# Kernel optimization log

Hardware: AMD Instinct MI355X
Metric: run time of the kernel (lower is better)

Reference implementation:

```python
import jax, jax.numpy as jnp
import numpy as np

HID = 1024
NH = 16
HD = HID // NH  # 64


def _lin_params(key, fan_in, fan_out):
    k1, k2 = jax.random.split(key)
    lim = 1.0 / np.sqrt(fan_in)
    W = jax.random.uniform(k1, (fan_in, fan_out), jnp.float32, -lim, lim)
    b = jax.random.uniform(k2, (fan_out,), jnp.float32, -lim, lim)
    return W, b


def setup_inputs() -> dict:
    key = jax.random.key(0)
    ks = jax.random.split(key, 12)
    B, S = 4, 1024
    inp = {
        'query': jax.random.normal(ks[0], (B, S, HID), jnp.float32),
        'key': jax.random.normal(ks[1], (B, S, HID), jnp.float32),
        'value': jax.random.normal(ks[2], (B, S, HID), jnp.float32),
    }
    inp['Wq'], inp['bq'] = _lin_params(ks[3], HID, HID)
    inp['Wk'], inp['bk'] = _lin_params(ks[4], HID, HID)
    inp['Wv'], inp['bv'] = _lin_params(ks[5], HID, HID)
    inp['Wp'], inp['bp'] = _lin_params(ks[6], HID, HID)
    inp['Wup'], inp['bup'] = _lin_params(ks[7], HD, 1)
    inp['Wud'], inp['bud'] = _lin_params(ks[8], HD, 1)
    inp['Wus'], inp['bus'] = _lin_params(ks[9], HID, NH)
    inp['Wo'], inp['bo'] = _lin_params(ks[10], HID, HID)
    return inp


def _split_heads(x, B, S):
    # [B,S,HID] -> [B,NH,S,HD]
    return x.reshape(B, S, NH, HD).transpose(0, 2, 1, 3)


def reference(query, key, value, Wq, bq, Wk, bk, Wv, bv, Wp, bp,
              Wup, bup, Wud, bud, Wus, bus, Wo, bo):
    B, S, _ = query.shape
    len_q = S

    q = query @ Wq + bq   # [B,S,HID]
    k = key @ Wk + bk
    v = value @ Wv + bv

    # Gaussian-window positional bias (per head, per query position)
    p = _split_heads(q @ Wp + bp, B, S)              # [B,NH,S,HD]
    tp = jnp.tanh(p)
    p_i = tp @ Wup + bup                             # [B,NH,S,1]
    z_i = tp @ Wud + bud                             # [B,NH,S,1]
    cen_pos = len_q * jax.nn.sigmoid(p_i)            # [B,NH,S,1]
    win_size = len_q * jax.nn.sigmoid(z_i)           # [B,NH,S,1]
    pos = jnp.arange(len_q, dtype=q.dtype)[None, None, None, :]  # [1,1,1,S]
    bias = (pos - cen_pos) ** 2 / (0.5 * win_size ** 2)          # [B,NH,S,S]

    # per-head alpha gate from raw query
    alpha = jax.nn.sigmoid(query @ Wus + bus)        # [B,S,NH]
    alpha = alpha.reshape(B, S, NH, 1).transpose(0, 2, 1, 3)  # [B,NH,S,1]

    qh = _split_heads(q, B, S)
    kh = _split_heads(k, B, S)
    vh = _split_heads(v, B, S)

    scale = 1.0 / jnp.sqrt(jnp.asarray(HD, q.dtype))
    scores = jnp.einsum('bhqd,bhkd->bhqk', qh, kh) * scale
    scores = scores - alpha * bias                   # inject gated Gaussian bias
    attn = jax.nn.softmax(scores, axis=-1)           # [B,NH,S,S]

    out = jnp.einsum('bhqk,bhkd->bhqd', attn, vh)    # [B,NH,S,HD]
    x = out.transpose(0, 2, 1, 3).reshape(B, S, HID)
    x = x @ Wo + bo
    return x, attn
```

## Files before the change

### kernel.cpp

```cpp
#include <hip/hip_runtime.h>
#include <hip/hip_bf16.h>
#include <math.h>

#define S_LEN 1024
#define HIDN  1024
#define NHEAD 16
#define HDIM  64
#define BATCH 4
#define MTOT  (BATCH * S_LEN)

typedef __attribute__((ext_vector_type(8))) short          bf16v8;
typedef __attribute__((ext_vector_type(8))) unsigned short u16v8;
typedef __attribute__((ext_vector_type(4))) unsigned short u16v4;
typedef __attribute__((ext_vector_type(4))) float          f32v4;

__device__ __forceinline__ unsigned short f2bf_rne(float x) {
    unsigned int u = __float_as_uint(x);
    unsigned int r = (u + 0x7fffu + ((u >> 16) & 1u)) >> 16;
    return (unsigned short)r;
}
__device__ __forceinline__ float bf2f(unsigned short h) {
    return __uint_as_float(((unsigned int)h) << 16);
}
__device__ __forceinline__ void split2(float x, unsigned short& h, unsigned short& l) {
    h = f2bf_rne(x);
    l = f2bf_rne(x - bf2f(h));
}

__global__ __launch_bounds__(256) void split_a(
    const float* __restrict__ X, unsigned short* __restrict__ H,
    unsigned short* __restrict__ L)
{
    const int i = blockIdx.x * 256 + threadIdx.x;
    const float4 x0 = ((const float4*)X)[2 * i];
    const float4 x1 = ((const float4*)X)[2 * i + 1];
    float xs[8] = {x0.x, x0.y, x0.z, x0.w, x1.x, x1.y, x1.z, x1.w};
    u16v8 h, l;
#pragma unroll
    for (int j = 0; j < 8; ++j) {
        unsigned short hh, ll;
        split2(xs[j], hh, ll);
        h[j] = hh; l[j] = ll;
    }
    ((u16v8*)H)[i] = h;
    ((u16v8*)L)[i] = l;
}

__global__ __launch_bounds__(256) void split_w(
    const float* __restrict__ W, unsigned short* __restrict__ H,
    unsigned short* __restrict__ L)
{
    __shared__ float T[64][65];
    const int t  = threadIdx.x;
    const int k0 = blockIdx.y * 64;
    const int n0 = blockIdx.x * 64;

    const int r = t >> 4;
    const int c = (t & 15) * 4;
#pragma unroll
    for (int i = 0; i < 4; ++i) {
        const int rr = r + i * 16;
        const float4 v = *(const float4*)&W[(size_t)(k0 + rr) * 1024 + n0 + c];
        T[rr][c + 0] = v.x; T[rr][c + 1] = v.y;
        T[rr][c + 2] = v.z; T[rr][c + 3] = v.w;
    }
    __syncthreads();

    const int n  = t >> 2;
    const int ko = (t & 3) * 16;
    u16v8 h0, h1, l0, l1;
#pragma unroll
    for (int kk = 0; kk < 8; ++kk) {
        unsigned short hh, ll;
        split2(T[ko + kk][n], hh, ll);
        h0[kk] = hh; l0[kk] = ll;
    }
#pragma unroll
    for (int kk = 0; kk < 8; ++kk) {
        unsigned short hh, ll;
        split2(T[ko + 8 + kk][n], hh, ll);
        h1[kk] = hh; l1[kk] = ll;
    }
    unsigned short* Hp = &H[(size_t)(n0 + n) * 1024 + k0 + ko];
    unsigned short* Lp = &L[(size_t)(n0 + n) * 1024 + k0 + ko];
    *(u16v8*)(Hp)     = h0;
    *(u16v8*)(Hp + 8) = h1;
    *(u16v8*)(Lp)     = l0;
    *(u16v8*)(Lp + 8) = l1;
}

__global__ __launch_bounds__(256) void gemm_bf16x3(
    const unsigned short* __restrict__ Ah, const unsigned short* __restrict__ Al,
    const unsigned short* __restrict__ Bh, const unsigned short* __restrict__ Bl,
    const float* __restrict__ bias, float* __restrict__ Cf,
    unsigned short* __restrict__ Ch, unsigned short* __restrict__ Cl, int vt)
{
    __shared__ short Ash[128][40];
    __shared__ short Asl[128][40];
    __shared__ short Bsh[128][40];
    __shared__ short Bsl[128][40];

    const int t    = threadIdx.x;
    const int bm   = blockIdx.y * 128;
    const int bn   = blockIdx.x * 128;
    const int lane = t & 63;
    const int w    = t >> 6;
    const int wr   = w >> 1;
    const int wc   = w & 1;
    const int fr   = lane & 15;
    const int fq   = lane >> 4;
    const int ks   = fq * 8;

    f32v4 zero = {0.f, 0.f, 0.f, 0.f};
    f32v4 acc[4][4];
#pragma unroll
    for (int i = 0; i < 4; ++i)
#pragma unroll
        for (int j = 0; j < 4; ++j) acc[i][j] = zero;

    const int sr = t >> 1;
    const int sc = (t & 1) * 16;
    const unsigned short* pAh = &Ah[(size_t)(bm + sr) * 1024 + sc];
    const unsigned short* pAl = &Al[(size_t)(bm + sr) * 1024 + sc];
    const unsigned short* pBh = &Bh[(size_t)(bn + sr) * 1024 + sc];
    const unsigned short* pBl = &Bl[(size_t)(bn + sr) * 1024 + sc];

    u16v8 rah0, rah1, ral0, ral1, rbh0, rbh1, rbl0, rbl1;
    auto LOAD = [&](int k0) {
        rah0 = *(const u16v8*)(pAh + k0);
        rah1 = *(const u16v8*)(pAh + k0 + 8);
        ral0 = *(const u16v8*)(pAl + k0);
        ral1 = *(const u16v8*)(pAl + k0 + 8);
        rbh0 = *(const u16v8*)(pBh + k0);
        rbh1 = *(const u16v8*)(pBh + k0 + 8);
        rbl0 = *(const u16v8*)(pBl + k0);
        rbl1 = *(const u16v8*)(pBl + k0 + 8);
    };

    LOAD(0);
    for (int k0 = 0; k0 < 1024; k0 += 32) {
        __syncthreads();
        *(u16v8*)&Ash[sr][sc]     = rah0;
        *(u16v8*)&Ash[sr][sc + 8] = rah1;
        *(u16v8*)&Asl[sr][sc]     = ral0;
        *(u16v8*)&Asl[sr][sc + 8] = ral1;
        *(u16v8*)&Bsh[sr][sc]     = rbh0;
        *(u16v8*)&Bsh[sr][sc + 8] = rbh1;
        *(u16v8*)&Bsl[sr][sc]     = rbl0;
        *(u16v8*)&Bsl[sr][sc + 8] = rbl1;
        __syncthreads();

        if (k0 + 32 < 1024) LOAD(k0 + 32);

        bf16v8 fah[4], fal[4], fbh[4], fbl[4];
#pragma unroll
        for (int i = 0; i < 4; ++i) {
            fah[i] = *(const bf16v8*)&Ash[wr * 64 + i * 16 + fr][ks];
            fal[i] = *(const bf16v8*)&Asl[wr * 64 + i * 16 + fr][ks];
            fbh[i] = *(const bf16v8*)&Bsh[wc * 64 + i * 16 + fr][ks];
            fbl[i] = *(const bf16v8*)&Bsl[wc * 64 + i * 16 + fr][ks];
        }
#pragma unroll
        for (int i = 0; i < 4; ++i)
#pragma unroll
            for (int j = 0; j < 4; ++j) {
                acc[i][j] = __builtin_amdgcn_mfma_f32_16x16x32_bf16(
                    fah[i], fbh[j], acc[i][j], 0, 0, 0);
                acc[i][j] = __builtin_amdgcn_mfma_f32_16x16x32_bf16(
                    fah[i], fbl[j], acc[i][j], 0, 0, 0);
                acc[i][j] = __builtin_amdgcn_mfma_f32_16x16x32_bf16(
                    fal[i], fbh[j], acc[i][j], 0, 0, 0);
            }
    }

#pragma unroll
    for (int j = 0; j < 4; ++j) {
        const int col = bn + wc * 64 + j * 16 + fr;
        const float bb = bias[col];
#pragma unroll
        for (int i = 0; i < 4; ++i) {
            const int row0 = bm + wr * 64 + i * 16 + fq * 4;
            const f32v4 cv = acc[i][j];
            if (vt) {
                u16v4 h4, l4;
#pragma unroll
                for (int r = 0; r < 4; ++r) {
                    unsigned short hh, ll;
                    split2(cv[r] + bb, hh, ll);
                    h4[r] = hh; l4[r] = ll;
                }
                const size_t base =
                    ((size_t)((row0 >> 10) * 16 + (col >> 6)) * 64 + (col & 63)) * 1024
                    + (row0 & 1023);
                *(u16v4*)&Ch[base] = h4;
                *(u16v4*)&Cl[base] = l4;
            } else {
#pragma unroll
                for (int r = 0; r < 4; ++r) {
                    const float v = cv[r] + bb;
                    const size_t idx = (size_t)(row0 + r) * 1024 + col;
                    if (Cf) Cf[idx] = v;
                    if (Ch) {
                        unsigned short hh, ll;
                        split2(v, hh, ll);
                        Ch[idx] = hh; Cl[idx] = ll;
                    }
                }
            }
        }
    }
}

__global__ __launch_bounds__(256) void alpha_kernel(
    const float* __restrict__ X, const float* __restrict__ Wus,
    const float* __restrict__ bus, float* __restrict__ alpha)
{
    __shared__ float Ws[1024 * 16];
    const int t = threadIdx.x;
#pragma unroll
    for (int i = 0; i < 16; ++i) {
        const int idx = t + i * 256;
        *reinterpret_cast<float4*>(&Ws[idx * 4]) =
            *reinterpret_cast<const float4*>(&Wus[idx * 4]);
    }
    __syncthreads();

    const int r = t >> 4, c = t & 15;
    const size_t row = (size_t)blockIdx.x * 16 + r;
    const float* x = &X[row * 1024];
    float acc = 0.f;
    for (int kk = 0; kk < 1024; kk += 4) {
        const float4 xv = *reinterpret_cast<const float4*>(&x[kk]);
        acc = fmaf(xv.x, Ws[(kk + 0) * 16 + c], acc);
        acc = fmaf(xv.y, Ws[(kk + 1) * 16 + c], acc);
        acc = fmaf(xv.z, Ws[(kk + 2) * 16 + c], acc);
        acc = fmaf(xv.w, Ws[(kk + 3) * 16 + c], acc);
    }
    acc += bus[c];
    alpha[row * 16 + c] = 1.f / (1.f + expf(-acc));
}

__global__ __launch_bounds__(256) void posparam_kernel(
    const float* __restrict__ p, const float* __restrict__ alpha,
    const float* __restrict__ Wup, const float* __restrict__ bup,
    const float* __restrict__ Wud, const float* __restrict__ bud,
    float* __restrict__ cen, float* __restrict__ c0)
{
    __shared__ float wu[64], wd[64];
    const int t = threadIdx.x;
    if (t < 64) { wu[t] = Wup[t]; wd[t] = Wud[t]; }
    __syncthreads();

    const int tid = blockIdx.x * 256 + t;
    const int b = tid >> 14;
    const int h = (tid >> 10) & 15;
    const int s = tid & 1023;

    const float* pr = &p[((size_t)(b * 1024 + s)) * 1024 + h * 64];
    float ap = 0.f, az = 0.f;
#pragma unroll
    for (int d = 0; d < 64; d += 4) {
        const float4 pv = *reinterpret_cast<const float4*>(&pr[d]);
        const float t0 = tanhf(pv.x), t1 = tanhf(pv.y);
        const float t2 = tanhf(pv.z), t3 = tanhf(pv.w);
        ap += t0 * wu[d] + t1 * wu[d + 1] + t2 * wu[d + 2] + t3 * wu[d + 3];
        az += t0 * wd[d] + t1 * wd[d + 1] + t2 * wd[d + 2] + t3 * wd[d + 3];
    }
    ap += bup[0];
    az += bud[0];
    const float cenv = 1024.f / (1.f + expf(-ap));
    const float win  = 1024.f / (1.f + expf(-az));
    const float al   = alpha[(size_t)(b * 1024 + s) * 16 + h];
    const int oi = (b * 16 + h) * 1024 + s;
    cen[oi] = cenv;
    c0[oi]  = al * 2.f / (win * win);
}

#define M0_SHIFT 8.0f
__global__ __launch_bounds__(256, 2) void attn_fused(
    const unsigned short* __restrict__ qh, const unsigned short* __restrict__ ql,
    const unsigned short* __restrict__ kh, const unsigned short* __restrict__ kl,
    const unsigned short* __restrict__ vTh, const unsigned short* __restrict__ vTl,
    const float* __restrict__ cen, const float* __restrict__ c0,
    float* __restrict__ attn,
    unsigned short* __restrict__ oh, unsigned short* __restrict__ ol)
{
    __shared__ unsigned short KH[64][64], KL[64][64];
    __shared__ unsigned short VH[64][64], VL[64][64];
    __shared__ unsigned short PH[128][64], PL[128][64];
    __shared__ float CEN[128], C0S[128];
    __shared__ float LSUM[2][128];
    __shared__ float RINV[128];

    const int bid   = blockIdx.x;
    const int z     = ((bid >> 6) << 3) | (bid & 7);
    const int itile = (bid >> 3) & 7;
    const int i0    = itile * 128;
    const int bq    = z >> 4;
    const int hd    = z & 15;

    const int t    = threadIdx.x;
    const int lane = t & 63;
    const int w    = t >> 6;
    const int wr   = w >> 1, wc = w & 1;
    const int fr   = lane & 15, fq = lane >> 4;

    if (t < 128) {
        CEN[t] = cen[(size_t)z * 1024 + i0 + t];
        C0S[t] = c0[(size_t)z * 1024 + i0 + t];
    }

    bf16v8 qfh_[4][2], qfl_[4][2];
#pragma unroll
    for (int i = 0; i < 4; ++i)
#pragma unroll
        for (int kk = 0; kk < 2; ++kk) {
            const size_t qa = (size_t)(bq * 1024 + i0 + wr * 64 + i * 16 + fr) * 1024
                              + hd * 64 + kk * 32 + fq * 8;
            qfh_[i][kk] = *(const bf16v8*)&qh[qa];
            qfl_[i][kk] = *(const bf16v8*)&ql[qa];
        }

    float lsum[4][4];
#pragma unroll
    for (int i = 0; i < 4; ++i)
#pragma unroll
        for (int r = 0; r < 4; ++r) lsum[i][r] = 0.f;

    const f32v4 zero = {0.f, 0.f, 0.f, 0.f};

    for (int jt = 0; jt < 16; ++jt) {
        const int j0 = jt * 64;
        __syncthreads();
#pragma unroll
        for (int pp = 0; pp < 2; ++pp) {
            const int c   = t + pp * 256;
            const int row = c >> 3;
            const int seg = c & 7;
            const size_t ga = (size_t)(bq * 1024 + j0 + row) * 1024 + hd * 64 + seg * 8;
            const int sl = (seg ^ (row & 7)) * 8;
            *(u16v8*)&KH[row][sl] = *(const u16v8*)&kh[ga];
            *(u16v8*)&KL[row][sl] = *(const u16v8*)&kl[ga];
        }
        __syncthreads();

        f32v4 acc[4][2];
#pragma unroll
        for (int i = 0; i < 4; ++i)
#pragma unroll
            for (int j2 = 0; j2 < 2; ++j2) acc[i][j2] = zero;

#pragma unroll
        for (int kk = 0; kk < 2; ++kk) {
            bf16v8 fbh[2], fbl[2];
#pragma unroll
            for (int j2 = 0; j2 < 2; ++j2) {
                const int rb = wc * 32 + j2 * 16 + fr;
                const int sb = ((kk * 4 + fq) ^ (rb & 7)) * 8;
                fbh[j2] = *(const bf16v8*)&KH[rb][sb];
                fbl[j2] = *(const bf16v8*)&KL[rb][sb];
            }
#pragma unroll
            for (int i = 0; i < 4; ++i)
#pragma unroll
                for (int j2 = 0; j2 < 2; ++j2) {
                    acc[i][j2] = __builtin_amdgcn_mfma_f32_16x16x32_bf16(
                        qfh_[i][kk], fbh[j2], acc[i][j2], 0, 0, 0);
                    acc[i][j2] = __builtin_amdgcn_mfma_f32_16x16x32_bf16(
                        qfh_[i][kk], fbl[j2], acc[i][j2], 0, 0, 0);
                    acc[i][j2] = __builtin_amdgcn_mfma_f32_16x16x32_bf16(
                        qfl_[i][kk], fbh[j2], acc[i][j2], 0, 0, 0);
                }
        }

#pragma unroll
        for (int i = 0; i < 4; ++i)
#pragma unroll
            for (int r = 0; r < 4; ++r) {
                const int row = wr * 64 + i * 16 + fq * 4 + r;
                const float cv = CEN[row], cc = C0S[row];
                float al = 0.f;
#pragma unroll
                for (int j2 = 0; j2 < 2; ++j2) {
                    const int col = wc * 32 + j2 * 16 + fr;
                    const float dd = (float)(j0 + col) - cv;
                    const float s  = acc[i][j2][r] * 0.125f - cc * dd * dd;
                    al += __expf(s - M0_SHIFT);
                }
                lsum[i][r] += al;
            }
    }

#pragma unroll
    for (int i = 0; i < 4; ++i)
#pragma unroll
        for (int r = 0; r < 4; ++r) {
            float v = lsum[i][r];
            v += __shfl_xor(v, 1);
            v += __shfl_xor(v, 2);
            v += __shfl_xor(v, 4);
            v += __shfl_xor(v, 8);
            if (fr == 0) LSUM[wc][wr * 64 + i * 16 + fq * 4 + r] = v;
        }
    __syncthreads();
    if (t < 128) RINV[t] = 1.f / (LSUM[0][t] + LSUM[1][t]);

    f32v4 acco[4][2];
#pragma unroll
    for (int i = 0; i < 4; ++i)
#pragma unroll
        for (int j = 0; j < 2; ++j) acco[i][j] = zero;

    float* attnZ = attn + (size_t)z * 1024 * 1024;
    const unsigned short* vhb = vTh + (size_t)z * 64 * 1024;
    const unsigned short* vlb = vTl + (size_t)z * 64 * 1024;

    for (int jt = 0; jt < 16; ++jt) {
        const int j0 = jt * 64;
        __syncthreads();
#pragma unroll
        for (int pp = 0; pp < 2; ++pp) {
            const int c   = t + pp * 256;
            const int row = c >> 3;
            const int seg = c & 7;
            const size_t ga = (size_t)(bq * 1024 + j0 + row) * 1024 + hd * 64 + seg * 8;
            const int sl = (seg ^ (row & 7)) * 8;
            *(u16v8*)&KH[row][sl] = *(const u16v8*)&kh[ga];
            *(u16v8*)&KL[row][sl] = *(const u16v8*)&kl[ga];
            const size_t va = (size_t)row * 1024 + j0 + seg * 8;
            *(u16v8*)&VH[row][sl] = *(const u16v8*)&vhb[va];
            *(u16v8*)&VL[row][sl] = *(const u16v8*)&vlb[va];
        }
        __syncthreads();

        f32v4 acc[4][2];
#pragma unroll
        for (int i = 0; i < 4; ++i)
#pragma unroll
            for (int j2 = 0; j2 < 2; ++j2) acc[i][j2] = zero;

#pragma unroll
        for (int kk = 0; kk < 2; ++kk) {
            bf16v8 fbh[2], fbl[2];
#pragma unroll
            for (int j2 = 0; j2 < 2; ++j2) {
                const int rb = wc * 32 + j2 * 16 + fr;
                const int sb = ((kk * 4 + fq) ^ (rb & 7)) * 8;
                fbh[j2] = *(const bf16v8*)&KH[rb][sb];
                fbl[j2] = *(const bf16v8*)&KL[rb][sb];
            }
#pragma unroll
            for (int i = 0; i < 4; ++i)
#pragma unroll
                for (int j2 = 0; j2 < 2; ++j2) {
                    acc[i][j2] = __builtin_amdgcn_mfma_f32_16x16x32_bf16(
                        qfh_[i][kk], fbh[j2], acc[i][j2], 0, 0, 0);
                    acc[i][j2] = __builtin_amdgcn_mfma_f32_16x16x32_bf16(
                        qfh_[i][kk], fbl[j2], acc[i][j2], 0, 0, 0);
                    acc[i][j2] = __builtin_amdgcn_mfma_f32_16x16x32_bf16(
                        qfl_[i][kk], fbh[j2], acc[i][j2], 0, 0, 0);
                }
        }

#pragma unroll
        for (int i = 0; i < 4; ++i)
#pragma unroll
            for (int r = 0; r < 4; ++r) {
                const int row = wr * 64 + i * 16 + fq * 4 + r;
                const float cv = CEN[row], cc = C0S[row], ri = RINV[row];
#pragma unroll
                for (int j2 = 0; j2 < 2; ++j2) {
                    const int col = wc * 32 + j2 * 16 + fr;
                    const float dd = (float)(j0 + col) - cv;
                    const float s  = acc[i][j2][r] * 0.125f - cc * dd * dd;
                    const float p  = __expf(s - M0_SHIFT) * ri;
                    attnZ[(size_t)(i0 + row) * 1024 + j0 + col] = p;
                    unsigned short hv, lv;
                    split2(p, hv, lv);
                    const int slot = ((col >> 3) ^ (row & 7)) * 8 + (col & 7);
                    PH[row][slot] = hv;
                    PL[row][slot] = lv;
                }
            }
        __syncthreads();

#pragma unroll
        for (int kk = 0; kk < 2; ++kk) {
            bf16v8 pah[4], pal[4], fbh[2], fbl[2];
#pragma unroll
            for (int iq = 0; iq < 4; ++iq) {
                const int rp = wr * 64 + iq * 16 + fr;
                const int sp = ((kk * 4 + fq) ^ (rp & 7)) * 8;
                pah[iq] = *(const bf16v8*)&PH[rp][sp];
                pal[iq] = *(const bf16v8*)&PL[rp][sp];
            }
#pragma unroll
            for (int jd = 0; jd < 2; ++jd) {
                const int rb = wc * 32 + jd * 16 + fr;
                const int sb = ((kk * 4 + fq) ^ (rb & 7)) * 8;
                fbh[jd] = *(const bf16v8*)&VH[rb][sb];
                fbl[jd] = *(const bf16v8*)&VL[rb][sb];
            }
#pragma unroll
            for (int iq = 0; iq < 4; ++iq)
#pragma unroll
                for (int jd = 0; jd < 2; ++jd) {
                    acco[iq][jd] = __builtin_amdgcn_mfma_f32_16x16x32_bf16(
                        pah[iq], fbh[jd], acco[iq][jd], 0, 0, 0);
                    acco[iq][jd] = __builtin_amdgcn_mfma_f32_16x16x32_bf16(
                        pah[iq], fbl[jd], acco[iq][jd], 0, 0, 0);
                    acco[iq][jd] = __builtin_amdgcn_mfma_f32_16x16x32_bf16(
                        pal[iq], fbh[jd], acco[iq][jd], 0, 0, 0);
                }
        }
    }

#pragma unroll
    for (int jd = 0; jd < 2; ++jd) {
        const int dcol = wc * 32 + jd * 16 + fr;
#pragma unroll
        for (int iq = 0; iq < 4; ++iq) {
            const int row0 = i0 + wr * 64 + iq * 16 + fq * 4;
            const f32v4 cv = acco[iq][jd];
#pragma unroll
            for (int r = 0; r < 4; ++r) {
                unsigned short hv, lv;
                split2(cv[r], hv, lv);
                const size_t idx = (size_t)(bq * 1024 + row0 + r) * 1024 + hd * 64 + dcol;
                oh[idx] = hv;
                ol[idx] = lv;
            }
        }
    }
}

extern "C" void kernel_launch(void* const* d_in, const int* in_sizes, int n_in,
                              void* d_out, int out_size, void* d_ws, size_t ws_size,
                              hipStream_t stream)
{
    const float* query = (const float*)d_in[0];
    const float* key_  = (const float*)d_in[1];
    const float* value = (const float*)d_in[2];
    const float* Wq  = (const float*)d_in[3];
    const float* bq  = (const float*)d_in[4];
    const float* Wk  = (const float*)d_in[5];
    const float* bk  = (const float*)d_in[6];
    const float* Wv  = (const float*)d_in[7];
    const float* bv  = (const float*)d_in[8];
    const float* Wp  = (const float*)d_in[9];
    const float* bp  = (const float*)d_in[10];
    const float* Wup = (const float*)d_in[11];
    const float* bup = (const float*)d_in[12];
    const float* Wud = (const float*)d_in[13];
    const float* bud = (const float*)d_in[14];
    const float* Wus = (const float*)d_in[15];
    const float* bus = (const float*)d_in[16];
    const float* Wo  = (const float*)d_in[17];
    const float* bo  = (const float*)d_in[18];

    float* x_out = (float*)d_out;
    float* attn  = x_out + (size_t)MTOT * HIDN;

    char* wsb = (char*)d_ws;
    unsigned short* qh  = (unsigned short*)(wsb);
    unsigned short* ql  = (unsigned short*)(wsb + (8u  << 20));
    unsigned short* kh  = (unsigned short*)(wsb + (16u << 20));
    unsigned short* kl  = (unsigned short*)(wsb + (24u << 20));
    unsigned short* vTh = (unsigned short*)(wsb + (32u << 20));
    unsigned short* vTl = (unsigned short*)(wsb + (40u << 20));
    float* p_ws  = (float*)(wsb + (48u << 20));
    unsigned short* oh = (unsigned short*)(wsb + (48u << 20));
    unsigned short* ol = (unsigned short*)(wsb + (56u << 20));
    float* alpha_ws = (float*)(wsb + (64u << 20));
    float* cen_ws   = (float*)(wsb + (64u << 20) + (256u << 10));
    float* c0_ws    = (float*)(wsb + (64u << 20) + (512u << 10));
    unsigned short* ah = (unsigned short*)attn;
    unsigned short* al = ah + (size_t)MTOT * HIDN;
    unsigned short* wh = al + (size_t)MTOT * HIDN;
    unsigned short* wl = wh + (size_t)HIDN * HIDN;
    unsigned short* w2h = qh;
    unsigned short* w2l = ql;

    const dim3 blk(256);
    const dim3 gsplit_a(MTOT * HIDN / 8 / 256);
    const dim3 gsplit_w(16, 16);
    const dim3 ggemm(HIDN / 128, MTOT / 128);

    split_w<<<gsplit_w, blk, 0, stream>>>(Wq, wh, wl);
    split_a<<<gsplit_a, blk, 0, stream>>>(query, ah, al);
    gemm_bf16x3<<<ggemm, blk, 0, stream>>>(ah, al, wh, wl, bq, nullptr, qh, ql, 0);
    split_w<<<gsplit_w, blk, 0, stream>>>(Wk, wh, wl);
    split_a<<<gsplit_a, blk, 0, stream>>>(key_, ah, al);
    gemm_bf16x3<<<ggemm, blk, 0, stream>>>(ah, al, wh, wl, bk, nullptr, kh, kl, 0);
    split_w<<<gsplit_w, blk, 0, stream>>>(Wv, wh, wl);
    split_a<<<gsplit_a, blk, 0, stream>>>(value, ah, al);
    gemm_bf16x3<<<ggemm, blk, 0, stream>>>(ah, al, wh, wl, bv, nullptr, vTh, vTl, 1);
    split_w<<<gsplit_w, blk, 0, stream>>>(Wp, wh, wl);
    gemm_bf16x3<<<ggemm, blk, 0, stream>>>(qh, ql, wh, wl, bp, p_ws, nullptr, nullptr, 0);
    alpha_kernel<<<dim3(MTOT / 16), blk, 0, stream>>>(query, Wus, bus, alpha_ws);
    posparam_kernel<<<dim3((BATCH * NHEAD * S_LEN) / 256), blk, 0, stream>>>(
        p_ws, alpha_ws, Wup, bup, Wud, bud, cen_ws, c0_ws);
    attn_fused<<<dim3(512), blk, 0, stream>>>(
        qh, ql, kh, kl, vTh, vTl, cen_ws, c0_ws, attn, oh, ol);
    split_w<<<gsplit_w, blk, 0, stream>>>(Wo, w2h, w2l);
    gemm_bf16x3<<<ggemm, blk, 0, stream>>>(oh, ol, w2h, w2l, bo, x_out,
                                           nullptr, nullptr, 0);
}
```

Measured before the change: 440.6 us.

## Compute transposed score tiles per wave to keep softmax rows in registers

Reorganizes the attention kernel so each wave owns 32 query rows and computes S^T = K·Q^T, putting each query row in a lane. Row sums then need only two cross-lane shuffles, with no shared-memory LSUM/RINV/CEN staging or block syncs for the softmax. The P tile stays in a per-wave LDS slice, which removes a block-wide barrier before P·V, and attention probabilities and outputs are written as float4/u16v4 vectors. The shared-memory cut permits raising launch bounds to 3 blocks per SM, at the cost of more register pressure and different store coalescing patterns.

New measurement: 456.2 us. 1.04x slower.

```diff
diff --git a/kernel.cpp b/kernel.cpp
--- a/kernel.cpp
+++ b/kernel.cpp
@@ -277,7 +277,7 @@
 }
 
 #define M0_SHIFT 8.0f
-__global__ __launch_bounds__(256, 2) void attn_fused(
+__global__ __launch_bounds__(256, 3) void attn_fused(
     const unsigned short* __restrict__ qh, const unsigned short* __restrict__ ql,
     const unsigned short* __restrict__ kh, const unsigned short* __restrict__ kl,
     const unsigned short* __restrict__ vTh, const unsigned short* __restrict__ vTl,
@@ -287,10 +287,7 @@
 {
     __shared__ unsigned short KH[64][64], KL[64][64];
     __shared__ unsigned short VH[64][64], VL[64][64];
-    __shared__ unsigned short PH[128][64], PL[128][64];
-    __shared__ float CEN[128], C0S[128];
-    __shared__ float LSUM[2][128];
-    __shared__ float RINV[128];
+    __shared__ unsigned short PTH[4][16][64], PTL[4][16][64];
 
     const int bid   = blockIdx.x;
     const int z     = ((bid >> 6) << 3) | (bid & 7);
@@ -302,32 +299,30 @@
     const int t    = threadIdx.x;
     const int lane = t & 63;
     const int w    = t >> 6;
-    const int wr   = w >> 1, wc = w & 1;
     const int fr   = lane & 15, fq = lane >> 4;
-
-    if (t < 128) {
-        CEN[t] = cen[(size_t)z * 1024 + i0 + t];
-        C0S[t] = c0[(size_t)z * 1024 + i0 + t];
-    }
-
-    bf16v8 qfh_[4][2], qfl_[4][2];
-#pragma unroll
-    for (int i = 0; i < 4; ++i)
+    const int q0w  = w * 32;
+
+    float cenq[2], c0q[2];
+#pragma unroll
+    for (int n2 = 0; n2 < 2; ++n2) {
+        const size_t ix = (size_t)z * 1024 + i0 + q0w + n2 * 16 + fr;
+        cenq[n2] = cen[ix];
+        c0q[n2]  = c0[ix];
+    }
+
+    bf16v8 qfh_[2][2], qfl_[2][2];
+#pragma unroll
+    for (int n2 = 0; n2 < 2; ++n2)
 #pragma unroll
         for (int kk = 0; kk < 2; ++kk) {
-            const size_t qa = (size_t)(bq * 1024 + i0 + wr * 64 + i * 16 + fr) * 1024
+            const size_t qa = (size_t)(bq * 1024 + i0 + q0w + n2 * 16 + fr) * 1024
                               + hd * 64 + kk * 32 + fq * 8;
-            qfh_[i][kk] = *(const bf16v8*)&qh[qa];
-            qfl_[i][kk] = *(const bf16v8*)&ql[qa];
-        }
-
-    float lsum[4][4];
-#pragma unroll
-    for (int i = 0; i < 4; ++i)
-#pragma unroll
-        for (int r = 0; r < 4; ++r) lsum[i][r] = 0.f;
+            qfh_[n2][kk] = *(const bf16v8*)&qh[qa];
+            qfl_[n2][kk] = *(const bf16v8*)&ql[qa];
+        }
 
     const f32v4 zero = {0.f, 0.f, 0.f, 0.f};
+    float lsum[2] = {0.f, 0.f};
 
     for (int jt = 0; jt < 16; ++jt) {
         const int j0 = jt * 64;
@@ -344,72 +339,65 @@
         }
         __syncthreads();
 
-        f32v4 acc[4][2];
-#pragma unroll
-        for (int i = 0; i < 4; ++i)
-#pragma unroll
-            for (int j2 = 0; j2 < 2; ++j2) acc[i][j2] = zero;
+        f32v4 accT[4][2];
+#pragma unroll
+        for (int mi = 0; mi < 4; ++mi)
+#pragma unroll
+            for (int n2 = 0; n2 < 2; ++n2) accT[mi][n2] = zero;
 
 #pragma unroll
         for (int kk = 0; kk < 2; ++kk) {
-            bf16v8 fbh[2], fbl[2];
-#pragma unroll
-            for (int j2 = 0; j2 < 2; ++j2) {
-                const int rb = wc * 32 + j2 * 16 + fr;
-                const int sb = ((kk * 4 + fq) ^ (rb & 7)) * 8;
-                fbh[j2] = *(const bf16v8*)&KH[rb][sb];
-                fbl[j2] = *(const bf16v8*)&KL[rb][sb];
-            }
-#pragma unroll
-            for (int i = 0; i < 4; ++i)
-#pragma unroll
-                for (int j2 = 0; j2 < 2; ++j2) {
-                    acc[i][j2] = __builtin_amdgcn_mfma_f32_16x16x32_bf16(
-                        qfh_[i][kk], fbh[j2], acc[i][j2], 0, 0, 0);
-                    acc[i][j2] = __builtin_amdgcn_mfma_f32_16x16x32_bf16(
-                        qfh_[i][kk], fbl[j2], acc[i][j2], 0, 0, 0);
-                    acc[i][j2] = __builtin_amdgcn_mfma_f32_16x16x32_bf16(
-                        qfl_[i][kk], fbh[j2], acc[i][j2], 0, 0, 0);
-                }
-        }
-
-#pragma unroll
-        for (int i = 0; i < 4; ++i)
-#pragma unroll
-            for (int r = 0; r < 4; ++r) {
-                const int row = wr * 64 + i * 16 + fq * 4 + r;
-                const float cv = CEN[row], cc = C0S[row];
+            bf16v8 kfh[4], kfl[4];
+#pragma unroll
+            for (int mi = 0; mi < 4; ++mi) {
+                const int ra = mi * 16 + fr;
+                const int sa = ((kk * 4 + fq) ^ (ra & 7)) * 8;
+                kfh[mi] = *(const bf16v8*)&KH[ra][sa];
+                kfl[mi] = *(const bf16v8*)&KL[ra][sa];
+            }
+#pragma unroll
+            for (int mi = 0; mi < 4; ++mi)
+#pragma unroll
+                for (int n2 = 0; n2 < 2; ++n2) {
+                    accT[mi][n2] = __builtin_amdgcn_mfma_f32_16x16x32_bf16(
+                        kfh[mi], qfh_[n2][kk], accT[mi][n2], 0, 0, 0);
+                    accT[mi][n2] = __builtin_amdgcn_mfma_f32_16x16x32_bf16(
+                        kfh[mi], qfl_[n2][kk], accT[mi][n2], 0, 0, 0);
+                    accT[mi][n2] = __builtin_amdgcn_mfma_f32_16x16x32_bf16(
+                        kfl[mi], qfh_[n2][kk], accT[mi][n2], 0, 0, 0);
+                }
+        }
+
+#pragma unroll
+        for (int mi = 0; mi < 4; ++mi)
+#pragma unroll
+            for (int n2 = 0; n2 < 2; ++n2) {
                 float al = 0.f;
 #pragma unroll
-                for (int j2 = 0; j2 < 2; ++j2) {
-                    const int col = wc * 32 + j2 * 16 + fr;
-                    const float dd = (float)(j0 + col) - cv;
-                    const float s  = acc[i][j2][r] * 0.125f - cc * dd * dd;
+                for (int r = 0; r < 4; ++r) {
+                    const int j = j0 + mi * 16 + fq * 4 + r;
+                    const float dd = (float)j - cenq[n2];
+                    const float s  = accT[mi][n2][r] * 0.125f - c0q[n2] * dd * dd;
                     al += __expf(s - M0_SHIFT);
                 }
-                lsum[i][r] += al;
-            }
-    }
-
-#pragma unroll
-    for (int i = 0; i < 4; ++i)
-#pragma unroll
-        for (int r = 0; r < 4; ++r) {
-            float v = lsum[i][r];
-            v += __shfl_xor(v, 1);
-            v += __shfl_xor(v, 2);
-            v += __shfl_xor(v, 4);
-            v += __shfl_xor(v, 8);
-            if (fr == 0) LSUM[wc][wr * 64 + i * 16 + fq * 4 + r] = v;
-        }
-    __syncthreads();
-    if (t < 128) RINV[t] = 1.f / (LSUM[0][t] + LSUM[1][t]);
-
-    f32v4 acco[4][2];
-#pragma unroll
-    for (int i = 0; i < 4; ++i)
-#pragma unroll
-        for (int j = 0; j < 2; ++j) acco[i][j] = zero;
+                lsum[n2] += al;
+            }
+    }
+
+    float rinv[2];
+#pragma unroll
+    for (int n2 = 0; n2 < 2; ++n2) {
+        float v = lsum[n2];
+        v += __shfl_xor(v, 16);
+        v += __shfl_xor(v, 32);
+        rinv[n2] = 1.f / v;
+    }
+
+    f32v4 accO[4][2];
+#pragma unroll
+    for (int mi = 0; mi < 4; ++mi)
+#pragma unroll
+        for (int n2 = 0; n2 < 2; ++n2) accO[mi][n2] = zero;
 
     float* attnZ = attn + (size_t)z * 1024 * 1024;
     const unsigned short* vhb = vTh + (size_t)z * 64 * 1024;
@@ -433,103 +421,98 @@
         }
         __syncthreads();
 
-        f32v4 acc[4][2];
-#pragma unroll
-        for (int i = 0; i < 4; ++i)
-#pragma unroll
-            for (int j2 = 0; j2 < 2; ++j2) acc[i][j2] = zero;
+        f32v4 accT[4][2];
+#pragma unroll
+        for (int mi = 0; mi < 4; ++mi)
+#pragma unroll
+            for (int n2 = 0; n2 < 2; ++n2) accT[mi][n2] = zero;
 
 #pragma unroll
         for (int kk = 0; kk < 2; ++kk) {
-            bf16v8 fbh[2], fbl[2];
-#pragma unroll
-            for (int j2 = 0; j2 < 2; ++j2) {
-                const int rb = wc * 32 + j2 * 16 + fr;
-                const int sb = ((kk * 4 + fq) ^ (rb & 7)) * 8;
-                fbh[j2] = *(const bf16v8*)&KH[rb][sb];
-                fbl[j2] = *(const bf16v8*)&KL[rb][sb];
-            }
-#pragma unroll
-            for (int i = 0; i < 4; ++i)
-#pragma unroll
-                for (int j2 = 0; j2 < 2; ++j2) {
-                    acc[i][j2] = __builtin_amdgcn_mfma_f32_16x16x32_bf16(
-                        qfh_[i][kk], fbh[j2], acc[i][j2], 0, 0, 0);
-                    acc[i][j2] = __builtin_amdgcn_mfma_f32_16x16x32_bf16(
-                        qfh_[i][kk], fbl[j2], acc[i][j2], 0, 0, 0);
-                    acc[i][j2] = __builtin_amdgcn_mfma_f32_16x16x32_bf16(
-                        qfl_[i][kk], fbh[j2], acc[i][j2], 0, 0, 0);
-                }
-        }
-
-#pragma unroll
-        for (int i = 0; i < 4; ++i)
-#pragma unroll
-            for (int r = 0; r < 4; ++r) {
-                const int row = wr * 64 + i * 16 + fq * 4 + r;
-                const float cv = CEN[row], cc = C0S[row], ri = RINV[row];
-#pragma unroll
-                for (int j2 = 0; j2 < 2; ++j2) {
-                    const int col = wc * 32 + j2 * 16 + fr;
-                    const float dd = (float)(j0 + col) - cv;
-                    const float s  = acc[i][j2][r] * 0.125f - cc * dd * dd;
+            bf16v8 kfh[4], kfl[4];
+#pragma unroll
+            for (int mi = 0; mi < 4; ++mi) {
+                const int ra = mi * 16 + fr;
+                const int sa = ((kk * 4 + fq) ^ (ra & 7)) * 8;
+                kfh[mi] = *(const bf16v8*)&KH[ra][sa];
+                kfl[mi] = *(const bf16v8*)&KL[ra][sa];
+            }
+#pragma unroll
+            for (int mi = 0; mi < 4; ++mi)
+#pragma unroll
+                for (int n2 = 0; n2 < 2; ++n2) {
+                    accT[mi][n2] = __builtin_amdgcn_mfma_f32_16x16x32_bf16(
+                        kfh[mi], qfh_[n2][kk], accT[mi][n2], 0, 0, 0);
+                    accT[mi][n2] = __builtin_amdgcn_mfma_f32_16x16x32_bf16(
+                        kfh[mi], qfl_[n2][kk], accT[mi][n2], 0, 0, 0);
+                    accT[mi][n2] = __builtin_amdgcn_mfma_f32_16x16x32_bf16(
+                        kfl[mi], qfh_[n2][kk], accT[mi][n2], 0, 0, 0);
+                }
+        }
+
+#pragma unroll
+        for (int n2 = 0; n2 < 2; ++n2) {
+            const float cv = cenq[n2], cc = c0q[n2], ri = rinv[n2];
+            const size_t arow = (size_t)(i0 + q0w + n2 * 16 + fr) * 1024 + j0;
+#pragma unroll
+            for (int mi = 0; mi < 4; ++mi) {
+                float4 pv4;
+                u16v4 h4, l4;
+#pragma unroll
+                for (int r = 0; r < 4; ++r) {
+                    const int j = j0 + mi * 16 + fq * 4 + r;
+                    const float dd = (float)j - cv;
+                    const float s  = accT[mi][n2][r] * 0.125f - cc * dd * dd;
                     const float p  = __expf(s - M0_SHIFT) * ri;
-                    attnZ[(size_t)(i0 + row) * 1024 + j0 + col] = p;
-                    unsigned short hv, lv;
-                    split2(p, hv, lv);
-                    const int slot = ((col >> 3) ^ (row & 7)) * 8 + (col & 7);
-                    PH[row][slot] = hv;
-                    PL[row][slot] = lv;
-                }
-            }
-        __syncthreads();
-
-#pragma unroll
-        for (int kk = 0; kk < 2; ++kk) {
-            bf16v8 pah[4], pal[4], fbh[2], fbl[2];
-#pragma unroll
-            for (int iq = 0; iq < 4; ++iq) {
-                const int rp = wr * 64 + iq * 16 + fr;
-                const int sp = ((kk * 4 + fq) ^ (rp & 7)) * 8;
-                pah[iq] = *(const bf16v8*)&PH[rp][sp];
-                pal[iq] = *(const bf16v8*)&PL[rp][sp];
-            }
-#pragma unroll
-            for (int jd = 0; jd < 2; ++jd) {
-                const int rb = wc * 32 + jd * 16 + fr;
-                const int sb = ((kk * 4 + fq) ^ (rb & 7)) * 8;
-                fbh[jd] = *(const bf16v8*)&VH[rb][sb];
-                fbl[jd] = *(const bf16v8*)&VL[rb][sb];
-            }
-#pragma unroll
-            for (int iq = 0; iq < 4; ++iq)
-#pragma unroll
-                for (int jd = 0; jd < 2; ++jd) {
-                    acco[iq][jd] = __builtin_amdgcn_mfma_f32_16x16x32_bf16(
-                        pah[iq], fbh[jd], acco[iq][jd], 0, 0, 0);
-                    acco[iq][jd] = __builtin_amdgcn_mfma_f32_16x16x32_bf16(
-                        pah[iq], fbl[jd], acco[iq][jd], 0, 0, 0);
-                    acco[iq][jd] = __builtin_amdgcn_mfma_f32_16x16x32_bf16(
-                        pal[iq], fbh[jd], acco[iq][jd], 0, 0, 0);
-                }
-        }
-    }
-
-#pragma unroll
-    for (int jd = 0; jd < 2; ++jd) {
-        const int dcol = wc * 32 + jd * 16 + fr;
-#pragma unroll
-        for (int iq = 0; iq < 4; ++iq) {
-            const int row0 = i0 + wr * 64 + iq * 16 + fq * 4;
-            const f32v4 cv = acco[iq][jd];
+                    ((float*)&pv4)[r] = p;
+                    unsigned short hh, ll;
+                    split2(p, hh, ll);
+                    h4[r] = hh; l4[r] = ll;
+                }
+                *(float4*)&attnZ[arow + mi * 16 + fq * 4] = pv4;
+                const int slot = (mi * 2 + (fq >> 1)) ^ (fr & 7);
+                const int off  = slot * 8 + (fq & 1) * 4;
+                *(u16v4*)&PTH[w][fr][off] = h4;
+                *(u16v4*)&PTL[w][fr][off] = l4;
+            }
+#pragma unroll
+            for (int kk = 0; kk < 2; ++kk) {
+                const int ps = ((kk * 4 + fq) ^ (fr & 7)) * 8;
+                const bf16v8 pfh = *(const bf16v8*)&PTH[w][fr][ps];
+                const bf16v8 pfl = *(const bf16v8*)&PTL[w][fr][ps];
+#pragma unroll
+                for (int mi = 0; mi < 4; ++mi) {
+                    const int rv = mi * 16 + fr;
+                    const int sv = ((kk * 4 + fq) ^ (rv & 7)) * 8;
+                    const bf16v8 vfh = *(const bf16v8*)&VH[rv][sv];
+                    const bf16v8 vfl = *(const bf16v8*)&VL[rv][sv];
+                    accO[mi][n2] = __builtin_amdgcn_mfma_f32_16x16x32_bf16(
+                        vfh, pfh, accO[mi][n2], 0, 0, 0);
+                    accO[mi][n2] = __builtin_amdgcn_mfma_f32_16x16x32_bf16(
+                        vfh, pfl, accO[mi][n2], 0, 0, 0);
+                    accO[mi][n2] = __builtin_amdgcn_mfma_f32_16x16x32_bf16(
+                        vfl, pfh, accO[mi][n2], 0, 0, 0);
+                }
+            }
+        }
+    }
+
+#pragma unroll
+    for (int n2 = 0; n2 < 2; ++n2) {
+        const size_t orow = (size_t)(bq * 1024 + i0 + q0w + n2 * 16 + fr) * 1024 + hd * 64;
+#pragma unroll
+        for (int mi = 0; mi < 4; ++mi) {
+            const f32v4 cv = accO[mi][n2];
+            u16v4 h4, l4;
 #pragma unroll
             for (int r = 0; r < 4; ++r) {
                 unsigned short hv, lv;
                 split2(cv[r], hv, lv);
-                const size_t idx = (size_t)(bq * 1024 + row0 + r) * 1024 + hd * 64 + dcol;
-                oh[idx] = hv;
-                ol[idx] = lv;
-            }
+                h4[r] = hv; l4[r] = lv;
+            }
+            const size_t idx = orow + mi * 16 + fq * 4;
+            *(u16v4*)&oh[idx] = h4;
+            *(u16v4*)&ol[idx] = l4;
         }
     }
 }
```
